# Optimization experiments

Measured on AMD Instinct MI355X. Metric: run time of the kernel, lower is better.

## Reference

```python
import jax, jax.numpy as jnp
import numpy as np
import math

B, C, H, W = 8, 64, 64, 64


def setup_inputs() -> dict:
    key = jax.random.key(0)
    k1, k2, k3, k4 = jax.random.split(key, 4)
    x = jax.random.normal(k1, (B, C, H, W), dtype=jnp.float32)
    fg_mask = jax.random.randint(k2, (B, 1, H, W), 0, 2, dtype=jnp.int32)
    w_qkv = jax.random.normal(k3, (3 * C, C), dtype=jnp.float32) * (1.0 / math.sqrt(C))
    w_proj = jax.random.normal(k4, (C, C), dtype=jnp.float32) * (1.0 / math.sqrt(C))
    b_proj = jnp.zeros((C,), dtype=jnp.float32)
    return {"x": x, "fg_mask": fg_mask, "w_qkv": w_qkv, "w_proj": w_proj, "b_proj": b_proj}


def reference(x, fg_mask, w_qkv, w_proj, b_proj):
    b, c, h, w = x.shape
    n = h * w
    # [B,C,H,W] -> [B,N,C]
    x_flat = x.reshape(b, c, n).transpose(0, 2, 1)
    qkv = x_flat @ w_qkv.T                      # [B,N,3C]
    q, k, v = jnp.split(qkv, 3, axis=-1)        # each [B,N,C]
    attn = jnp.einsum('bnc,bmc->bnm', q, k) / math.sqrt(c)  # [B,N,N]
    fg = fg_mask.reshape(b, n)                  # [B,N]
    attn = jnp.where(fg[:, None, :] == 0, -jnp.inf, attn)
    attn = jax.nn.softmax(attn, axis=-1)
    out = attn @ v                              # [B,N,C]
    out = out @ w_proj.T + b_proj               # [B,N,C]
    return out.transpose(0, 2, 1).reshape(b, c, h, w)
```

## Files before the change

kernel.cpp:

```cpp
#include <hip/hip_runtime.h>
#include <math.h>

#define Bdim 8
#define Cdim 64
#define Ndim 4096
#define TK   32
#define GNT  32

typedef __bf16 bf16x8 __attribute__((ext_vector_type(8)));
typedef __bf16 bf16x4 __attribute__((ext_vector_type(4)));
typedef float  f32x4  __attribute__((ext_vector_type(4)));

__device__ __forceinline__ void gload_lds16(const void* g, void* l) {
    __builtin_amdgcn_global_load_lds(
        (const __attribute__((address_space(1))) void*)g,
        (__attribute__((address_space(3))) void*)l, 16, 0, 0);
}

__device__ __forceinline__ float fexp2(float x) {
#if __has_builtin(__builtin_amdgcn_exp2f)
    return __builtin_amdgcn_exp2f(x);
#else
    return exp2f(x);
#endif
}

__global__ __launch_bounds__(256) void wconv_kernel(
    const float* __restrict__ w, __bf16* __restrict__ whi, __bf16* __restrict__ wlo)
{
    const int i = blockIdx.x * 256 + threadIdx.x;
    const float v = w[i];
    const __bf16 h = (__bf16)v;
    whi[i] = h;
    wlo[i] = (__bf16)(v - (float)h);
}

__global__ __launch_bounds__(256) void qkv_mfma_kernel(
    const float* __restrict__ x,
    const __bf16* __restrict__ whi, const __bf16* __restrict__ wlo,
    __bf16* __restrict__ Qb, __bf16* __restrict__ Kb, __bf16* __restrict__ Vb)
{
    __shared__ __align__(16) __bf16 tr[4][16 * 64];

    const int bx   = blockIdx.x;
    const int b    = bx >> 6;
    const int nblk = bx & 63;
    const int tid  = threadIdx.x;
    const int wv   = tid >> 6;
    const int l    = tid & 63;
    const int g    = l >> 4;
    const int li   = l & 15;
    const int nbase = nblk * 64 + wv * 16;

    const float KS = 0.125f * 1.44269504089f;

    bf16x8 xhi[2], xlo[2];
#pragma unroll
    for (int kc = 0; kc < 2; ++kc)
#pragma unroll
        for (int jj = 0; jj < 8; ++jj) {
            const int c = kc * 32 + 8 * g + jj;
            const float v = x[((size_t)(b * 64 + c)) * Ndim + nbase + li];
            const __bf16 h = (__bf16)v;
            xhi[kc][jj] = h;
            xlo[kc][jj] = (__bf16)(v - (float)h);
        }

    __bf16* trw = tr[wv];

#pragma unroll
    for (int jt = 0; jt < 12; ++jt) {
        const int j = 16 * jt + li;
        const __bf16* wh = whi + j * 64;
        const __bf16* wl = wlo + j * 64;
        const bf16x8 ah0 = *(const bf16x8*)(wh + 8 * g);
        const bf16x8 ah1 = *(const bf16x8*)(wh + 32 + 8 * g);
        const bf16x8 al0 = *(const bf16x8*)(wl + 8 * g);
        const bf16x8 al1 = *(const bf16x8*)(wl + 32 + 8 * g);
        f32x4 d = (f32x4){0.f, 0.f, 0.f, 0.f};
        d = __builtin_amdgcn_mfma_f32_16x16x32_bf16(ah0, xhi[0], d, 0, 0, 0);
        d = __builtin_amdgcn_mfma_f32_16x16x32_bf16(ah1, xhi[1], d, 0, 0, 0);
        d = __builtin_amdgcn_mfma_f32_16x16x32_bf16(ah0, xlo[0], d, 0, 0, 0);
        d = __builtin_amdgcn_mfma_f32_16x16x32_bf16(ah1, xlo[1], d, 0, 0, 0);
        d = __builtin_amdgcn_mfma_f32_16x16x32_bf16(al0, xhi[0], d, 0, 0, 0);
        d = __builtin_amdgcn_mfma_f32_16x16x32_bf16(al1, xhi[1], d, 0, 0, 0);

        if (jt < 8) {
            const int   jt3 = jt & 3;
            const float qs  = (jt < 4) ? KS : 1.f;
            bf16x4 pk;
#pragma unroll
            for (int r = 0; r < 4; ++r) pk[r] = (__bf16)(d[r] * qs);
            const int gran = (2 * jt3 + (g >> 1)) ^ (li & 7);
            *(bf16x4*)(trw + li * 64 + gran * 8 + 4 * (g & 1)) = pk;

            if (jt3 == 3) {
                __bf16* dstm = ((jt < 4) ? Qb : Kb)
                             + ((size_t)b * Ndim + nbase) * 64;
#pragma unroll
                for (int p = 0; p < 2; ++p) {
                    const int row = p * 8 + (l >> 3);
                    const uint4 vr = *(const uint4*)(
                        trw + row * 64 + ((l & 7) ^ (l >> 3)) * 8);
                    *(uint4*)(dstm + row * 64 + 8 * (l & 7)) = vr;
                }
            }
        } else {
#pragma unroll
            for (int r = 0; r < 4; ++r) {
                const int cv = (jt - 8) * 16 + 4 * g + r;
                Vb[((size_t)(b * 64 + cv)) * Ndim + nbase + li] = (__bf16)d[r];
            }
        }
    }
}

__global__ __launch_bounds__(512, 4) void attn_kernel(
    const __bf16* __restrict__ Qb, const __bf16* __restrict__ Kb,
    const __bf16* __restrict__ Vb, const int* __restrict__ fg,
    const float* __restrict__ w_proj, const float* __restrict__ b_proj,
    float* __restrict__ out)
{
    __shared__ __align__(16) __bf16 kt[4][2][TK * 64];
    __shared__ __align__(16) __bf16 vt[4][2][64 * TK];
    __shared__ __align__(16) float  mtf[4][2][TK];

    const int bx   = blockIdx.x;
    const int b    = bx >> 6;
    const int qblk = bx & 63;
    const int tid  = threadIdx.x;
    const int wv   = tid >> 6;
    const int grp  = wv >> 1;
    const int wsub = wv & 1;
    const int l    = tid & 63;
    const int g    = l >> 4;
    const int li   = l & 15;

    const int qlo = qblk * 64 + wsub * 32 + li;
    const __bf16* qb_lo = Qb + ((size_t)b * Ndim + qlo) * 64;
    const bf16x8 qa0 = *(const bf16x8*)(qb_lo + 8 * g);
    const bf16x8 qa1 = *(const bf16x8*)(qb_lo + 32 + 8 * g);
    const bf16x8 qa2 = *(const bf16x8*)(qb_lo + 16 * 64 + 8 * g);
    const bf16x8 qa3 = *(const bf16x8*)(qb_lo + 16 * 64 + 32 + 8 * g);

    const int kbase0 = grp * 1024;
    const __bf16* ksrcc[2];
    const __bf16* vsrcc[2];
    int kdst[2], vdst[2];
#pragma unroll
    for (int c = 0; c < 2; ++c) {
        const int R  = wsub * 16 + c * 8 + (l >> 3);
        const int kk = 8 * ((R >> 2) & 3) + 4 * (R >> 4) + (R & 3);
        ksrcc[c] = Kb + ((size_t)b * Ndim + kbase0 + kk) * 64 + 8 * ((l & 7) ^ (R & 7));
        kdst[c]  = (wsub * 16 + c * 8) * 64;
        const int row = wsub * 32 + c * 16 + (l >> 2);
        vsrcc[c] = Vb + ((size_t)(b * 64 + row)) * Ndim + kbase0
                 + 8 * ((l & 3) ^ ((row >> 1) & 3));
        vdst[c]  = (wsub * 32 + c * 16) * TK;
    }
    const int* fgp = fg + b * Ndim + kbase0;

    auto stage = [&](int t, int buf) {
#pragma unroll
        for (int c = 0; c < 2; ++c)
            gload_lds16(ksrcc[c] + (size_t)t * (TK * 64), &kt[grp][buf][kdst[c]]);
#pragma unroll
        for (int c = 0; c < 2; ++c)
            gload_lds16(vsrcc[c] + t * TK, &vt[grp][buf][vdst[c]]);
        if (wsub == 0 && l < TK)
            mtf[grp][buf][l] = fgp[t * TK + l] ? -12.f : -1e30f;
    };

    f32x4 accl[4], acch[4];
#pragma unroll
    for (int ct = 0; ct < 4; ++ct) {
        accl[ct] = (f32x4){0.f, 0.f, 0.f, 0.f};
        acch[ct] = (f32x4){0.f, 0.f, 0.f, 0.f};
    }
    f32x4 psv_l = (f32x4){0.f, 0.f, 0.f, 0.f};
    f32x4 psv_h = (f32x4){0.f, 0.f, 0.f, 0.f};

    stage(0, 0);

    for (int it = 0; it < GNT; ++it) {
        const int buf = it & 1;
        __syncthreads();
        if (it + 1 < GNT) stage(it + 1, buf ^ 1);

        const f32x4 mb0 = *(const f32x4*)(&mtf[grp][buf][8 * g]);
        const f32x4 mb1 = *(const f32x4*)(&mtf[grp][buf][8 * g + 4]);

        f32x4 s2l[2], s2h[2];
        __builtin_amdgcn_s_setprio(1);
#pragma unroll
        for (int st = 0; st < 2; ++st) {
            const int rb = (16 * st + li) * 64;
            const int sw = li & 7;
            const bf16x8 kb0 = *(const bf16x8*)(&kt[grp][buf][rb + 8 * (g ^ sw)]);
            const bf16x8 kb1 = *(const bf16x8*)(&kt[grp][buf][rb + 8 * ((4 + g) ^ sw)]);
            f32x4 zl = st ? mb1 : mb0;
            zl = __builtin_amdgcn_mfma_f32_16x16x32_bf16(kb0, qa0, zl, 0, 0, 0);
            zl = __builtin_amdgcn_mfma_f32_16x16x32_bf16(kb1, qa1, zl, 0, 0, 0);
            s2l[st] = zl;
            f32x4 zh = st ? mb1 : mb0;
            zh = __builtin_amdgcn_mfma_f32_16x16x32_bf16(kb0, qa2, zh, 0, 0, 0);
            zh = __builtin_amdgcn_mfma_f32_16x16x32_bf16(kb1, qa3, zh, 0, 0, 0);
            s2h[st] = zh;
        }
        __builtin_amdgcn_s_setprio(0);

#pragma unroll
        for (int st = 0; st < 2; ++st)
#pragma unroll
            for (int r = 0; r < 4; ++r) {
                const float el = fexp2(s2l[st][r]);
                const float eh = fexp2(s2h[st][r]);
                s2l[st][r] = el; psv_l[r] += el;
                s2h[st][r] = eh; psv_h[r] += eh;
            }

        bf16x8 pbl, pbh;
#pragma unroll
        for (int r = 0; r < 4; ++r) {
            pbl[r]     = (__bf16)s2l[0][r];
            pbl[4 + r] = (__bf16)s2l[1][r];
            pbh[r]     = (__bf16)s2h[0][r];
            pbh[4 + r] = (__bf16)s2h[1][r];
        }

        __builtin_amdgcn_s_setprio(1);
#pragma unroll
        for (int ct = 0; ct < 4; ++ct) {
            const int c = 16 * ct + li;
            const bf16x8 vf = *(const bf16x8*)(
                &vt[grp][buf][c * TK + 8 * (g ^ ((li >> 1) & 3))]);
            accl[ct] = __builtin_amdgcn_mfma_f32_16x16x32_bf16(vf, pbl, accl[ct], 0, 0, 0);
            acch[ct] = __builtin_amdgcn_mfma_f32_16x16x32_bf16(vf, pbh, acch[ct], 0, 0, 0);
        }
        __builtin_amdgcn_s_setprio(0);
    }

    float lsum_l = (psv_l[0] + psv_l[1]) + (psv_l[2] + psv_l[3]);
    float lsum_h = (psv_h[0] + psv_h[1]) + (psv_h[2] + psv_h[3]);
    lsum_l += __shfl_xor(lsum_l, 16);
    lsum_l += __shfl_xor(lsum_l, 32);
    lsum_h += __shfl_xor(lsum_h, 16);
    lsum_h += __shfl_xor(lsum_h, 32);

    float* mlb = (float*)&kt[0][0][0];
    __syncthreads();

    auto chunk = [&](int cidx) -> float* {
        return (cidx < 4) ? (float*)&vt[0][0][0] + cidx * 2048
                          : mlb + 256 + (cidx - 4) * 2048;
    };

    if (grp > 0) {
        const int p = grp - 1;
        if (g == 0) {
            mlb[((p * 2 + wsub) * 2 + 0) * 16 + li] = lsum_l;
            mlb[((p * 2 + wsub) * 2 + 1) * 16 + li] = lsum_h;
        }
        float* o = chunk(p * 2 + wsub);
#pragma unroll
        for (int fi = 0; fi < 8; ++fi)
            *(f32x4*)(o + (fi * 64 + l) * 4) = (fi < 4) ? accl[fi] : acch[fi - 4];
    }
    __syncthreads();
    if (grp > 0) return;

    float Ltl = lsum_l, Lth = lsum_h;
#pragma unroll
    for (int p = 0; p < 3; ++p) {
        Ltl += mlb[((p * 2 + wsub) * 2 + 0) * 16 + li];
        Lth += mlb[((p * 2 + wsub) * 2 + 1) * 16 + li];
    }
    const float invl = 1.f / Ltl, invh = 1.f / Lth;

    bf16x8 ob01l, ob23l, ob01h, ob23h;
#pragma unroll
    for (int fi = 0; fi < 8; ++fi) {
        const int  ct = fi & 3;
        const bool hi = fi >= 4;
        f32x4 s = hi ? acch[ct] : accl[ct];
#pragma unroll
        for (int p = 0; p < 3; ++p) {
            const f32x4 v = *(const f32x4*)(chunk(p * 2 + wsub) + (fi * 64 + l) * 4);
#pragma unroll
            for (int r = 0; r < 4; ++r) s[r] += v[r];
        }
        const float inv = hi ? invh : invl;
#pragma unroll
        for (int r = 0; r < 4; ++r) {
            const __bf16 o = (__bf16)(s[r] * inv);
            if (fi == 0) ob01l[r] = o;
            else if (fi == 1) ob01l[4 + r] = o;
            else if (fi == 2) ob23l[r] = o;
            else if (fi == 3) ob23l[4 + r] = o;
            else if (fi == 4) ob01h[r] = o;
            else if (fi == 5) ob01h[4 + r] = o;
            else if (fi == 6) ob23h[r] = o;
            else              ob23h[4 + r] = o;
        }
    }

    const int nbase = qblk * 64 + wsub * 32;
#pragma unroll
    for (int cot = 0; cot < 4; ++cot) {
        const int co = 16 * cot + li;
        const float* wr = w_proj + co * 64;
        const float4 f0 = *(const float4*)(wr + 4 * g);
        const float4 f1 = *(const float4*)(wr + 16 + 4 * g);
        const float4 f2 = *(const float4*)(wr + 32 + 4 * g);
        const float4 f3 = *(const float4*)(wr + 48 + 4 * g);
        bf16x8 wf0, wf1;
        wf0[0] = (__bf16)f0.x; wf0[1] = (__bf16)f0.y; wf0[2] = (__bf16)f0.z; wf0[3] = (__bf16)f0.w;
        wf0[4] = (__bf16)f1.x; wf0[5] = (__bf16)f1.y; wf0[6] = (__bf16)f1.z; wf0[7] = (__bf16)f1.w;
        wf1[0] = (__bf16)f2.x; wf1[1] = (__bf16)f2.y; wf1[2] = (__bf16)f2.z; wf1[3] = (__bf16)f2.w;
        wf1[4] = (__bf16)f3.x; wf1[5] = (__bf16)f3.y; wf1[6] = (__bf16)f3.z; wf1[7] = (__bf16)f3.w;

        f32x4 yl = (f32x4){0.f, 0.f, 0.f, 0.f};
        yl = __builtin_amdgcn_mfma_f32_16x16x32_bf16(wf0, ob01l, yl, 0, 0, 0);
        yl = __builtin_amdgcn_mfma_f32_16x16x32_bf16(wf1, ob23l, yl, 0, 0, 0);
        f32x4 yh = (f32x4){0.f, 0.f, 0.f, 0.f};
        yh = __builtin_amdgcn_mfma_f32_16x16x32_bf16(wf0, ob01h, yh, 0, 0, 0);
        yh = __builtin_amdgcn_mfma_f32_16x16x32_bf16(wf1, ob23h, yh, 0, 0, 0);

        const f32x4 bp = *(const f32x4*)(b_proj + 16 * cot + 4 * g);
#pragma unroll
        for (int r = 0; r < 4; ++r) {
            const int co_s = 16 * cot + 4 * g + r;
            float* orow = out + ((size_t)(b * 64 + co_s)) * Ndim + nbase;
            orow[li]      = yl[r] + bp[r];
            orow[16 + li] = yh[r] + bp[r];
        }
    }
}

extern "C" void kernel_launch(void* const* d_in, const int* in_sizes, int n_in,
                              void* d_out, int out_size, void* d_ws, size_t ws_size,
                              hipStream_t stream) {
    const float* x      = (const float*)d_in[0];
    const int*   fg     = (const int*)d_in[1];
    const float* w_qkv  = (const float*)d_in[2];
    const float* w_proj = (const float*)d_in[3];
    const float* b_proj = (const float*)d_in[4];
    float* out = (float*)d_out;

    const size_t per = (size_t)Bdim * Cdim * Ndim;
    __bf16* Qb  = (__bf16*)d_ws;
    __bf16* Kb  = Qb + per;
    __bf16* Vb  = Kb + per;
    __bf16* Whi = Vb + per;
    __bf16* Wlo = Whi + 3 * Cdim * Cdim;

    wconv_kernel<<<dim3(3 * Cdim * Cdim / 256), dim3(256), 0, stream>>>(
        w_qkv, Whi, Wlo);
    qkv_mfma_kernel<<<dim3(Bdim * (Ndim / 64)), dim3(256), 0, stream>>>(
        x, Whi, Wlo, Qb, Kb, Vb);
    attn_kernel<<<dim3(Bdim * (Ndim / 64)), dim3(512), 0, stream>>>(
        Qb, Kb, Vb, fg, w_proj, b_proj, out);
}
```

Baseline: 73.82 us.

## Fuse weight bf16 split into QKV kernel and split Q/K/V across blocks

Removes the separate weight-conversion kernel: each QKV block now loads its 64x64 slice of w_qkv, splits it into hi/lo bf16 in swizzled LDS, and computes only one of Q, K or V. The grid triples so each block does a third of the MFMA work, which adds parallelism, but every block now re-reads and converts the x tile and a weight slice. The attention kernel's block index mapping is also changed to interleave batches (b = bx & 7), which changes how work is distributed across CUs and caches.

Result: faster. 61.25 us (-17.0%).

```diff
diff --git a/kernel.cpp b/kernel.cpp
--- a/kernel.cpp
+++ b/kernel.cpp
@@ -25,26 +25,18 @@
 #endif
 }
 
-__global__ __launch_bounds__(256) void wconv_kernel(
-    const float* __restrict__ w, __bf16* __restrict__ whi, __bf16* __restrict__ wlo)
-{
-    const int i = blockIdx.x * 256 + threadIdx.x;
-    const float v = w[i];
-    const __bf16 h = (__bf16)v;
-    whi[i] = h;
-    wlo[i] = (__bf16)(v - (float)h);
-}
-
 __global__ __launch_bounds__(256) void qkv_mfma_kernel(
-    const float* __restrict__ x,
-    const __bf16* __restrict__ whi, const __bf16* __restrict__ wlo,
+    const float* __restrict__ x, const float* __restrict__ w_qkv,
     __bf16* __restrict__ Qb, __bf16* __restrict__ Kb, __bf16* __restrict__ Vb)
 {
+    __shared__ __align__(16) __bf16 whs[64 * 64];
+    __shared__ __align__(16) __bf16 wls[64 * 64];
     __shared__ __align__(16) __bf16 tr[4][16 * 64];
 
     const int bx   = blockIdx.x;
-    const int b    = bx >> 6;
-    const int nblk = bx & 63;
+    const int jc   = bx % 3;
+    const int nblk = (bx / 3) & 63;
+    const int b    = bx / 192;
     const int tid  = threadIdx.x;
     const int wv   = tid >> 6;
     const int l    = tid & 63;
@@ -54,6 +46,32 @@
 
     const float KS = 0.125f * 1.44269504089f;
 
+    {
+        const float* wsrc = w_qkv + jc * 4096 + tid * 16;
+        const float4 f0 = *(const float4*)(wsrc);
+        const float4 f1 = *(const float4*)(wsrc + 4);
+        const float4 f2 = *(const float4*)(wsrc + 8);
+        const float4 f3 = *(const float4*)(wsrc + 12);
+        const int row = tid >> 2;
+        const int gb  = (tid & 3) * 2;
+        bf16x8 h0, l0, h1, l1;
+        const float* fp[4] = {(const float*)&f0, (const float*)&f1,
+                              (const float*)&f2, (const float*)&f3};
+#pragma unroll
+        for (int q = 0; q < 2; ++q)
+#pragma unroll
+            for (int e = 0; e < 8; ++e) {
+                const float v = fp[q * 2 + (e >> 2)][e & 3];
+                const __bf16 h = (__bf16)v;
+                if (q == 0) { h0[e] = h; l0[e] = (__bf16)(v - (float)h); }
+                else        { h1[e] = h; l1[e] = (__bf16)(v - (float)h); }
+            }
+        *(bf16x8*)(whs + row * 64 + 8 * ((gb)     ^ (row & 7))) = h0;
+        *(bf16x8*)(whs + row * 64 + 8 * ((gb + 1) ^ (row & 7))) = h1;
+        *(bf16x8*)(wls + row * 64 + 8 * ((gb)     ^ (row & 7))) = l0;
+        *(bf16x8*)(wls + row * 64 + 8 * ((gb + 1) ^ (row & 7))) = l1;
+    }
+
     bf16x8 xhi[2], xlo[2];
 #pragma unroll
     for (int kc = 0; kc < 2; ++kc)
@@ -65,18 +83,19 @@
             xhi[kc][jj] = h;
             xlo[kc][jj] = (__bf16)(v - (float)h);
         }
+    __syncthreads();
 
     __bf16* trw = tr[wv];
-
-#pragma unroll
-    for (int jt = 0; jt < 12; ++jt) {
-        const int j = 16 * jt + li;
-        const __bf16* wh = whi + j * 64;
-        const __bf16* wl = wlo + j * 64;
-        const bf16x8 ah0 = *(const bf16x8*)(wh + 8 * g);
-        const bf16x8 ah1 = *(const bf16x8*)(wh + 32 + 8 * g);
-        const bf16x8 al0 = *(const bf16x8*)(wl + 8 * g);
-        const bf16x8 al1 = *(const bf16x8*)(wl + 32 + 8 * g);
+    const float qs = (jc == 0) ? KS : 1.f;
+
+#pragma unroll
+    for (int jt = 0; jt < 4; ++jt) {
+        const int rw = 16 * jt + li;
+        const int rs = li & 7;
+        const bf16x8 ah0 = *(const bf16x8*)(whs + rw * 64 + 8 * (g ^ rs));
+        const bf16x8 ah1 = *(const bf16x8*)(whs + rw * 64 + 8 * ((4 + g) ^ rs));
+        const bf16x8 al0 = *(const bf16x8*)(wls + rw * 64 + 8 * (g ^ rs));
+        const bf16x8 al1 = *(const bf16x8*)(wls + rw * 64 + 8 * ((4 + g) ^ rs));
         f32x4 d = (f32x4){0.f, 0.f, 0.f, 0.f};
         d = __builtin_amdgcn_mfma_f32_16x16x32_bf16(ah0, xhi[0], d, 0, 0, 0);
         d = __builtin_amdgcn_mfma_f32_16x16x32_bf16(ah1, xhi[1], d, 0, 0, 0);
@@ -85,32 +104,29 @@
         d = __builtin_amdgcn_mfma_f32_16x16x32_bf16(al0, xhi[0], d, 0, 0, 0);
         d = __builtin_amdgcn_mfma_f32_16x16x32_bf16(al1, xhi[1], d, 0, 0, 0);
 
-        if (jt < 8) {
-            const int   jt3 = jt & 3;
-            const float qs  = (jt < 4) ? KS : 1.f;
-            bf16x4 pk;
-#pragma unroll
-            for (int r = 0; r < 4; ++r) pk[r] = (__bf16)(d[r] * qs);
-            const int gran = (2 * jt3 + (g >> 1)) ^ (li & 7);
-            *(bf16x4*)(trw + li * 64 + gran * 8 + 4 * (g & 1)) = pk;
-
-            if (jt3 == 3) {
-                __bf16* dstm = ((jt < 4) ? Qb : Kb)
-                             + ((size_t)b * Ndim + nbase) * 64;
-#pragma unroll
-                for (int p = 0; p < 2; ++p) {
-                    const int row = p * 8 + (l >> 3);
-                    const uint4 vr = *(const uint4*)(
-                        trw + row * 64 + ((l & 7) ^ (l >> 3)) * 8);
-                    *(uint4*)(dstm + row * 64 + 8 * (l & 7)) = vr;
-                }
+        if (jc == 2) {
+#pragma unroll
+            for (int r = 0; r < 4; ++r) {
+                const int cv = jt * 16 + 4 * g + r;
+                Vb[((size_t)(b * 64 + cv)) * Ndim + nbase + li] = (__bf16)d[r];
             }
         } else {
-#pragma unroll
-            for (int r = 0; r < 4; ++r) {
-                const int cv = (jt - 8) * 16 + 4 * g + r;
-                Vb[((size_t)(b * 64 + cv)) * Ndim + nbase + li] = (__bf16)d[r];
-            }
+            bf16x4 pk;
+#pragma unroll
+            for (int r = 0; r < 4; ++r) pk[r] = (__bf16)(d[r] * qs);
+            const int gran = (2 * jt + (g >> 1)) ^ (li & 7);
+            *(bf16x4*)(trw + li * 64 + gran * 8 + 4 * (g & 1)) = pk;
+        }
+    }
+
+    if (jc != 2) {
+        __bf16* dstm = ((jc == 0) ? Qb : Kb) + ((size_t)b * Ndim + nbase) * 64;
+#pragma unroll
+        for (int p = 0; p < 2; ++p) {
+            const int row = p * 8 + (l >> 3);
+            const uint4 vr = *(const uint4*)(
+                trw + row * 64 + ((l & 7) ^ (l >> 3)) * 8);
+            *(uint4*)(dstm + row * 64 + 8 * (l & 7)) = vr;
         }
     }
 }
@@ -126,8 +142,8 @@
     __shared__ __align__(16) float  mtf[4][2][TK];
 
     const int bx   = blockIdx.x;
-    const int b    = bx >> 6;
-    const int qblk = bx & 63;
+    const int b    = bx & 7;
+    const int qblk = (bx >> 3) & 63;
     const int tid  = threadIdx.x;
     const int wv   = tid >> 6;
     const int grp  = wv >> 1;
@@ -348,16 +364,12 @@
     float* out = (float*)d_out;
 
     const size_t per = (size_t)Bdim * Cdim * Ndim;
-    __bf16* Qb  = (__bf16*)d_ws;
-    __bf16* Kb  = Qb + per;
-    __bf16* Vb  = Kb + per;
-    __bf16* Whi = Vb + per;
-    __bf16* Wlo = Whi + 3 * Cdim * Cdim;
-
-    wconv_kernel<<<dim3(3 * Cdim * Cdim / 256), dim3(256), 0, stream>>>(
-        w_qkv, Whi, Wlo);
-    qkv_mfma_kernel<<<dim3(Bdim * (Ndim / 64)), dim3(256), 0, stream>>>(
-        x, Whi, Wlo, Qb, Kb, Vb);
+    __bf16* Qb = (__bf16*)d_ws;
+    __bf16* Kb = Qb + per;
+    __bf16* Vb = Kb + per;
+
+    qkv_mfma_kernel<<<dim3(Bdim * (Ndim / 64) * 3), dim3(256), 0, stream>>>(
+        x, w_qkv, Qb, Kb, Vb);
     attn_kernel<<<dim3(Bdim * (Ndim / 64)), dim3(512), 0, stream>>>(
         Qb, Kb, Vb, fg, w_proj, b_proj, out);
 }
```
